# Kernel optimization log

Measured on AMD Instinct MI355X. Metric: run time of the kernel, lower is better.

The kernel has to match this reference:

```python
import jax, jax.numpy as jnp
import numpy as np
import math

NDIM = 16
SCALE = math.sqrt(1.0 / NDIM)


def setup_inputs() -> dict:
    key = jax.random.key(0)
    ks = jax.random.split(key, 7)
    L, Bsz, Dm = 4096, 4, 1024
    return {
        "x": jax.random.normal(ks[0], (L, Bsz, Dm), dtype=jnp.float32),
        "log_dt": jax.random.normal(ks[1], (Dm, 1), dtype=jnp.float32),
        "log_A_real": jax.random.normal(ks[2], (Dm, NDIM), dtype=jnp.float32),
        "A_imag": jax.random.normal(ks[3], (Dm, NDIM), dtype=jnp.float32),
        "B": jax.random.normal(ks[4], (Dm, NDIM, 2), dtype=jnp.float32),
        "C": jax.random.normal(ks[5], (Dm, NDIM, 2), dtype=jnp.float32),
        "D_param": jax.random.normal(ks[6], (Dm,), dtype=jnp.float32),
    }


def _compute_kernel(log_dt, log_A_real, A_imag, B, C, length):
    dt = jnp.exp(log_dt)                                  # (D,1)
    A = -jnp.exp(log_A_real) + 1j * A_imag                # (D,N) complex
    dtA = A * dt                                          # (D,N)
    Cc = (B[..., 0] + 1j * B[..., 1]) * (C[..., 0] + 1j * C[..., 1])  # (D,N)
    # bilinear discretization
    p = Cc * dt / (1.0 - dtA / 2)                         # (D,N)
    log_q = jnp.log((1.0 + dtA / 2) / (1.0 - dtA / 2))    # (D,N)
    # Vandermonde: (D,N,L) complex — the kernel-gen bottleneck
    vander = jnp.exp(jnp.arange(length)[None, None, :] * log_q[:, :, None])
    k = jnp.einsum('dnl,dn->dl', vander, p * SCALE).real  # (D,L)
    return k


def reference(x, log_dt, log_A_real, A_imag, B, C, D_param):
    seq_len, bsz, dim = x.shape
    residual = x * D_param                                # (L,B,D)
    xt = jnp.transpose(x, (1, 2, 0))                      # (B,D,L)
    k = _compute_kernel(log_dt, log_A_real, A_imag, B, C, seq_len)
    fft_len = 2 * seq_len
    k_f = jnp.fft.rfft(k.astype(jnp.float32), n=fft_len)  # (D, fft_len//2+1)
    x_f = jnp.fft.rfft(xt.astype(jnp.float32), n=fft_len)  # (B,D, fft_len//2+1)
    out = jnp.fft.irfft(x_f * k_f, n=fft_len)[..., :seq_len]  # (B,D,L)
    out = out.astype(x.dtype)
    return jax.nn.silu(jnp.transpose(out, (2, 0, 1)) + residual)
```

## Files before the change

### kernel.cpp

```cpp
#include <hip/hip_runtime.h>
#include <math.h>

#define L_SEQ  4096
#define BSZ    4
#define DM     1024
#define NS     16
#define NCHUNK 64
#define CHUNK  (L_SEQ / NCHUNK)
#define LOG2_CHUNK 6
#define SCALE  0.25f


__global__ void s4d_params(const float* __restrict__ log_dt,
                           const float* __restrict__ log_A_real,
                           const float* __restrict__ A_imag,
                           const float* __restrict__ Bp,
                           const float* __restrict__ Cp,
                           float4* __restrict__ pq) {
    int t = blockIdx.x * blockDim.x + threadIdx.x;
    if (t >= DM * NS) return;
    int d = t >> 4;
    float dt = expf(log_dt[d]);
    float Ar = -expf(log_A_real[t]);
    float Ai = A_imag[t];
    float ar = 0.5f * Ar * dt, ai = 0.5f * Ai * dt;
    float den_r = 1.0f - ar, den_i = -ai;
    float num_r = 1.0f + ar, num_i = ai;
    float inv = 1.0f / (den_r * den_r + den_i * den_i);
    float qr = (num_r * den_r + num_i * den_i) * inv;
    float qi = (num_i * den_r - num_r * den_i) * inv;
    float B0 = Bp[2 * t], B1 = Bp[2 * t + 1];
    float C0 = Cp[2 * t], C1 = Cp[2 * t + 1];
    float ccr = B0 * C0 - B1 * C1;
    float cci = B0 * C1 + B1 * C0;
    float s = dt * inv * SCALE;
    float pr = (ccr * den_r + cci * den_i) * s;
    float pi = (cci * den_r - ccr * den_i) * s;
    pq[t] = make_float4(qr, qi, pr, pi);
}

__global__ __launch_bounds__(256, 4)
void s4d_pass1(const float* __restrict__ x,
               const float4* __restrict__ pq,
               float2* __restrict__ S) {
    int tid = blockIdx.x * 256 + threadIdx.x;
    int d  = tid & (DM - 1);
    int bc = tid >> 10;
    int c  = bc & (NCHUNK - 1);
    int b  = bc >> LOG2_CHUNK;

    float qr[NS], qi[NS], hr[NS], hi[NS];
#pragma unroll
    for (int n = 0; n < NS; ++n) {
        float4 v = pq[d * NS + n];
        qr[n] = v.x; qi[n] = v.y; hr[n] = 0.0f; hi[n] = 0.0f;
    }
    const float* xp = x + (size_t)(c * CHUNK) * (BSZ * DM) + b * DM + d;
#pragma unroll 4
    for (int l = 0; l < CHUNK; ++l) {
        float xv = xp[(size_t)l * (BSZ * DM)];
#pragma unroll
        for (int n = 0; n < NS; ++n) {
            float nr = fmaf(qr[n], hr[n], fmaf(-qi[n], hi[n], xv));
            float ni = fmaf(qr[n], hi[n], qi[n] * hr[n]);
            hr[n] = nr; hi[n] = ni;
        }
    }
    float2* sp = S + ((size_t)bc * DM + d) * NS;
#pragma unroll
    for (int n = 0; n < NS; ++n) sp[n] = make_float2(hr[n], hi[n]);
}

__global__ void s4d_pass2(const float4* __restrict__ pq,
                          float2* __restrict__ S) {
    int tid = blockIdx.x * 256 + threadIdx.x;
    int n = tid & (NS - 1);
    int d = (tid >> 4) & (DM - 1);
    int b = tid >> 14;
    float4 v = pq[d * NS + n];
    float qr = v.x, qi = v.y;
#pragma unroll
    for (int i = 0; i < LOG2_CHUNK; ++i) {
        float nr = qr * qr - qi * qi;
        float ni = 2.0f * qr * qi;
        qr = nr; qi = ni;
    }
    float hr = 0.0f, hi = 0.0f;
    for (int c = 0; c < NCHUNK; ++c) {
        size_t idx = ((size_t)(b * NCHUNK + c) * DM + d) * NS + n;
        float2 s = S[idx];
        S[idx] = make_float2(hr, hi);
        float nr = fmaf(qr, hr, fmaf(-qi, hi, s.x));
        float ni = fmaf(qr, hi, fmaf(qi, hr, s.y));
        hr = nr; hi = ni;
    }
}

__global__ __launch_bounds__(256, 4)
void s4d_pass3(const float* __restrict__ x,
               const float* __restrict__ Dp,
               const float4* __restrict__ pq,
               const float2* __restrict__ S,
               float* __restrict__ out) {
    int tid = blockIdx.x * 256 + threadIdx.x;
    int d  = tid & (DM - 1);
    int bc = tid >> 10;
    int c  = bc & (NCHUNK - 1);
    int b  = bc >> LOG2_CHUNK;

    float qr[NS], qi[NS], pr[NS], pi[NS], hr[NS], hi[NS];
#pragma unroll
    for (int n = 0; n < NS; ++n) {
        float4 v = pq[d * NS + n];
        qr[n] = v.x; qi[n] = v.y; pr[n] = v.z; pi[n] = v.w;
    }
    const float2* sp = S + ((size_t)bc * DM + d) * NS;
#pragma unroll
    for (int n = 0; n < NS; ++n) {
        float2 s = sp[n];
        hr[n] = s.x; hi[n] = s.y;
    }
    float dpar = Dp[d];
    const float* xp = x + (size_t)(c * CHUNK) * (BSZ * DM) + b * DM + d;
    float* op = out + (size_t)(c * CHUNK) * (BSZ * DM) + b * DM + d;
#pragma unroll 4
    for (int l = 0; l < CHUNK; ++l) {
        float xv = xp[(size_t)l * (BSZ * DM)];
        float acc = 0.0f;
#pragma unroll
        for (int n = 0; n < NS; ++n) {
            float nr = fmaf(qr[n], hr[n], fmaf(-qi[n], hi[n], xv));
            float ni = fmaf(qr[n], hi[n], qi[n] * hr[n]);
            hr[n] = nr; hi[n] = ni;
            acc = fmaf(pr[n], nr, fmaf(-pi[n], ni, acc));
        }
        float z = fmaf(xv, dpar, acc);
        float sig = 1.0f / (1.0f + expf(-z));
        op[(size_t)l * (BSZ * DM)] = z * sig;
    }
}

extern "C" void kernel_launch(void* const* d_in, const int* in_sizes, int n_in,
                              void* d_out, int out_size, void* d_ws, size_t ws_size,
                              hipStream_t stream) {
    const float* x          = (const float*)d_in[0];
    const float* log_dt     = (const float*)d_in[1];
    const float* log_A_real = (const float*)d_in[2];
    const float* A_imag     = (const float*)d_in[3];
    const float* Bp         = (const float*)d_in[4];
    const float* Cp         = (const float*)d_in[5];
    const float* Dp         = (const float*)d_in[6];
    float* out = (float*)d_out;

    float4* pq = (float4*)d_ws;
    float2* S  = (float2*)((char*)d_ws + sizeof(float4) * DM * NS);

    hipLaunchKernelGGL(s4d_params, dim3((DM * NS) / 256), dim3(256), 0, stream,
                       log_dt, log_A_real, A_imag, Bp, Cp, pq);
    hipLaunchKernelGGL(s4d_pass1, dim3((BSZ * NCHUNK * DM) / 256), dim3(256), 0, stream,
                       x, pq, S);
    hipLaunchKernelGGL(s4d_pass2, dim3((BSZ * DM * NS) / 256), dim3(256), 0, stream,
                       pq, S);
    hipLaunchKernelGGL(s4d_pass3, dim3((BSZ * NCHUNK * DM) / 256), dim3(256), 0, stream,
                       x, Dp, pq, S, out);
}
```

Baseline: 224.3 us.

## Split SSM states across half-waves, transpose param/state layouts for coalescing

Each (b,chunk,d) scan in passes 1 and 3 is now split across two half-wavefronts, each handling 8 of the 16 states, with a cross-lane shuffle reducing the output contribution. Parameter and chunk-state buffers are transposed to an n-major layout so loads and stores are coalesced over d. Pass 2 gets its chunk loads batched and prefetched eight at a time. This doubles thread count and cuts per-thread register pressure and serial latency, but x is now loaded twice and half the lanes idle on the store.

```diff
diff --git a/kernel.cpp b/kernel.cpp
--- a/kernel.cpp
+++ b/kernel.cpp
@@ -5,10 +5,12 @@
 #define BSZ    4
 #define DM     1024
 #define NS     16
+#define NSH    8
 #define NCHUNK 64
 #define CHUNK  (L_SEQ / NCHUNK)
 #define LOG2_CHUNK 6
 #define SCALE  0.25f
+#define LBD    (BSZ * DM)
 
 
 __global__ void s4d_params(const float* __restrict__ log_dt,
@@ -16,127 +18,169 @@
                            const float* __restrict__ A_imag,
                            const float* __restrict__ Bp,
                            const float* __restrict__ Cp,
-                           float4* __restrict__ pq) {
+                           float2* __restrict__ qbuf,
+                           float2* __restrict__ pbuf) {
     int t = blockIdx.x * blockDim.x + threadIdx.x;
-    if (t >= DM * NS) return;
-    int d = t >> 4;
+    if (t >= NS * DM) return;
+    int n = t >> 10, d = t & (DM - 1);
+    int i = d * NS + n;
     float dt = expf(log_dt[d]);
-    float Ar = -expf(log_A_real[t]);
-    float Ai = A_imag[t];
+    float Ar = -expf(log_A_real[i]);
+    float Ai = A_imag[i];
     float ar = 0.5f * Ar * dt, ai = 0.5f * Ai * dt;
     float den_r = 1.0f - ar, den_i = -ai;
     float num_r = 1.0f + ar, num_i = ai;
     float inv = 1.0f / (den_r * den_r + den_i * den_i);
     float qr = (num_r * den_r + num_i * den_i) * inv;
     float qi = (num_i * den_r - num_r * den_i) * inv;
-    float B0 = Bp[2 * t], B1 = Bp[2 * t + 1];
-    float C0 = Cp[2 * t], C1 = Cp[2 * t + 1];
+    float B0 = Bp[2 * i], B1 = Bp[2 * i + 1];
+    float C0 = Cp[2 * i], C1 = Cp[2 * i + 1];
     float ccr = B0 * C0 - B1 * C1;
     float cci = B0 * C1 + B1 * C0;
     float s = dt * inv * SCALE;
     float pr = (ccr * den_r + cci * den_i) * s;
     float pi = (cci * den_r - ccr * den_i) * s;
-    pq[t] = make_float4(qr, qi, pr, pi);
+    qbuf[t] = make_float2(qr, qi);
+    pbuf[t] = make_float2(pr, pi);
 }
 
 __global__ __launch_bounds__(256, 4)
 void s4d_pass1(const float* __restrict__ x,
-               const float4* __restrict__ pq,
+               const float2* __restrict__ qbuf,
+               float2* __restrict__ S) {
+    int tid  = blockIdx.x * 256 + threadIdx.x;
+    int lane = tid & 63;
+    int dlo  = lane & 31;
+    int half = lane >> 5;
+    int u    = tid >> 6;
+    int dhi  = u & 31;
+    int bc   = u >> 5;
+    int c    = bc & (NCHUNK - 1);
+    int d    = dhi * 32 + dlo;
+    int b    = bc >> LOG2_CHUNK;
+    int nb   = half * NSH;
+
+    float qr[NSH], qi[NSH], hr[NSH], hi[NSH];
+#pragma unroll
+    for (int j = 0; j < NSH; ++j) {
+        float2 v = qbuf[(nb + j) * DM + d];
+        qr[j] = v.x; qi[j] = v.y; hr[j] = 0.0f; hi[j] = 0.0f;
+    }
+    const float* xp = x + (size_t)(c * CHUNK) * LBD + b * DM + d;
+#pragma unroll 4
+    for (int l = 0; l < CHUNK; ++l) {
+        float xv = xp[(size_t)l * LBD];
+#pragma unroll
+        for (int j = 0; j < NSH; ++j) {
+            float nr = fmaf(qr[j], hr[j], fmaf(-qi[j], hi[j], xv));
+            float ni = fmaf(qr[j], hi[j], qi[j] * hr[j]);
+            hr[j] = nr; hi[j] = ni;
+        }
+    }
+    float2* sp = S + ((size_t)bc * NS + nb) * DM + d;
+#pragma unroll
+    for (int j = 0; j < NSH; ++j) sp[(size_t)j * DM] = make_float2(hr[j], hi[j]);
+}
+
+__global__ __launch_bounds__(256)
+void s4d_pass2(const float2* __restrict__ qbuf,
                float2* __restrict__ S) {
     int tid = blockIdx.x * 256 + threadIdx.x;
-    int d  = tid & (DM - 1);
-    int bc = tid >> 10;
-    int c  = bc & (NCHUNK - 1);
-    int b  = bc >> LOG2_CHUNK;
-
-    float qr[NS], qi[NS], hr[NS], hi[NS];
-#pragma unroll
-    for (int n = 0; n < NS; ++n) {
-        float4 v = pq[d * NS + n];
-        qr[n] = v.x; qi[n] = v.y; hr[n] = 0.0f; hi[n] = 0.0f;
-    }
-    const float* xp = x + (size_t)(c * CHUNK) * (BSZ * DM) + b * DM + d;
-#pragma unroll 4
-    for (int l = 0; l < CHUNK; ++l) {
-        float xv = xp[(size_t)l * (BSZ * DM)];
-#pragma unroll
-        for (int n = 0; n < NS; ++n) {
-            float nr = fmaf(qr[n], hr[n], fmaf(-qi[n], hi[n], xv));
-            float ni = fmaf(qr[n], hi[n], qi[n] * hr[n]);
-            hr[n] = nr; hi[n] = ni;
-        }
-    }
-    float2* sp = S + ((size_t)bc * DM + d) * NS;
-#pragma unroll
-    for (int n = 0; n < NS; ++n) sp[n] = make_float2(hr[n], hi[n]);
-}
-
-__global__ void s4d_pass2(const float4* __restrict__ pq,
-                          float2* __restrict__ S) {
-    int tid = blockIdx.x * 256 + threadIdx.x;
-    int n = tid & (NS - 1);
-    int d = (tid >> 4) & (DM - 1);
+    int d = tid & (DM - 1);
+    int n = (tid >> 10) & (NS - 1);
     int b = tid >> 14;
-    float4 v = pq[d * NS + n];
-    float qr = v.x, qi = v.y;
+    float2 qv = qbuf[n * DM + d];
+    float qr = qv.x, qi = qv.y;
 #pragma unroll
     for (int i = 0; i < LOG2_CHUNK; ++i) {
         float nr = qr * qr - qi * qi;
         float ni = 2.0f * qr * qi;
         qr = nr; qi = ni;
     }
+    size_t base = ((size_t)b * NCHUNK * NS + n) * DM + d;
+    const size_t cs = (size_t)NS * DM;
     float hr = 0.0f, hi = 0.0f;
-    for (int c = 0; c < NCHUNK; ++c) {
-        size_t idx = ((size_t)(b * NCHUNK + c) * DM + d) * NS + n;
-        float2 s = S[idx];
-        S[idx] = make_float2(hr, hi);
-        float nr = fmaf(qr, hr, fmaf(-qi, hi, s.x));
-        float ni = fmaf(qr, hi, fmaf(qi, hr, s.y));
-        hr = nr; hi = ni;
+    float2 s0 = S[base + 0 * cs], s1 = S[base + 1 * cs],
+           s2 = S[base + 2 * cs], s3 = S[base + 3 * cs],
+           s4 = S[base + 4 * cs], s5 = S[base + 5 * cs],
+           s6 = S[base + 6 * cs], s7 = S[base + 7 * cs];
+#pragma unroll
+    for (int c0 = 0; c0 < NCHUNK; c0 += 8) {
+        float2 t0, t1, t2, t3, t4, t5, t6, t7;
+        if (c0 + 8 < NCHUNK) {
+            size_t nb2 = base + (size_t)(c0 + 8) * cs;
+            t0 = S[nb2 + 0 * cs]; t1 = S[nb2 + 1 * cs];
+            t2 = S[nb2 + 2 * cs]; t3 = S[nb2 + 3 * cs];
+            t4 = S[nb2 + 4 * cs]; t5 = S[nb2 + 5 * cs];
+            t6 = S[nb2 + 6 * cs]; t7 = S[nb2 + 7 * cs];
+        }
+#define STEP(J, SB)                                                      \
+        {                                                                \
+            S[base + (size_t)(c0 + J) * cs] = make_float2(hr, hi);       \
+            float nr = fmaf(qr, hr, fmaf(-qi, hi, SB.x));                \
+            float ni = fmaf(qr, hi, fmaf(qi, hr, SB.y));                 \
+            hr = nr; hi = ni;                                            \
+        }
+        STEP(0, s0) STEP(1, s1) STEP(2, s2) STEP(3, s3)
+        STEP(4, s4) STEP(5, s5) STEP(6, s6) STEP(7, s7)
+#undef STEP
+        if (c0 + 8 < NCHUNK) {
+            s0 = t0; s1 = t1; s2 = t2; s3 = t3;
+            s4 = t4; s5 = t5; s6 = t6; s7 = t7;
+        }
     }
 }
 
 __global__ __launch_bounds__(256, 4)
 void s4d_pass3(const float* __restrict__ x,
                const float* __restrict__ Dp,
-               const float4* __restrict__ pq,
+               const float2* __restrict__ qbuf,
+               const float2* __restrict__ pbuf,
                const float2* __restrict__ S,
                float* __restrict__ out) {
-    int tid = blockIdx.x * 256 + threadIdx.x;
-    int d  = tid & (DM - 1);
-    int bc = tid >> 10;
-    int c  = bc & (NCHUNK - 1);
-    int b  = bc >> LOG2_CHUNK;
-
-    float qr[NS], qi[NS], pr[NS], pi[NS], hr[NS], hi[NS];
-#pragma unroll
-    for (int n = 0; n < NS; ++n) {
-        float4 v = pq[d * NS + n];
-        qr[n] = v.x; qi[n] = v.y; pr[n] = v.z; pi[n] = v.w;
-    }
-    const float2* sp = S + ((size_t)bc * DM + d) * NS;
-#pragma unroll
-    for (int n = 0; n < NS; ++n) {
-        float2 s = sp[n];
-        hr[n] = s.x; hi[n] = s.y;
+    int tid  = blockIdx.x * 256 + threadIdx.x;
+    int lane = tid & 63;
+    int dlo  = lane & 31;
+    int half = lane >> 5;
+    int u    = tid >> 6;
+    int dhi  = u & 31;
+    int bc   = u >> 5;
+    int c    = bc & (NCHUNK - 1);
+    int d    = dhi * 32 + dlo;
+    int b    = bc >> LOG2_CHUNK;
+    int nb   = half * NSH;
+
+    float qr[NSH], qi[NSH], pr[NSH], pi[NSH], hr[NSH], hi[NSH];
+#pragma unroll
+    for (int j = 0; j < NSH; ++j) {
+        float2 v = qbuf[(nb + j) * DM + d];
+        float2 w = pbuf[(nb + j) * DM + d];
+        qr[j] = v.x; qi[j] = v.y; pr[j] = w.x; pi[j] = w.y;
+    }
+    const float2* sp = S + ((size_t)bc * NS + nb) * DM + d;
+#pragma unroll
+    for (int j = 0; j < NSH; ++j) {
+        float2 s = sp[(size_t)j * DM];
+        hr[j] = s.x; hi[j] = s.y;
     }
     float dpar = Dp[d];
-    const float* xp = x + (size_t)(c * CHUNK) * (BSZ * DM) + b * DM + d;
-    float* op = out + (size_t)(c * CHUNK) * (BSZ * DM) + b * DM + d;
-#pragma unroll 4
+    const float* xp = x + (size_t)(c * CHUNK) * LBD + b * DM + d;
+    float* op = out + (size_t)(c * CHUNK) * LBD + b * DM + d;
+#pragma unroll 2
     for (int l = 0; l < CHUNK; ++l) {
-        float xv = xp[(size_t)l * (BSZ * DM)];
+        float xv = xp[(size_t)l * LBD];
         float acc = 0.0f;
 #pragma unroll
-        for (int n = 0; n < NS; ++n) {
-            float nr = fmaf(qr[n], hr[n], fmaf(-qi[n], hi[n], xv));
-            float ni = fmaf(qr[n], hi[n], qi[n] * hr[n]);
-            hr[n] = nr; hi[n] = ni;
-            acc = fmaf(pr[n], nr, fmaf(-pi[n], ni, acc));
-        }
+        for (int j = 0; j < NSH; ++j) {
+            float nr = fmaf(qr[j], hr[j], fmaf(-qi[j], hi[j], xv));
+            float ni = fmaf(qr[j], hi[j], qi[j] * hr[j]);
+            hr[j] = nr; hi[j] = ni;
+            acc = fmaf(pr[j], nr, fmaf(-pi[j], ni, acc));
+        }
+        acc += __shfl_xor(acc, 32, 64);
         float z = fmaf(xv, dpar, acc);
         float sig = 1.0f / (1.0f + expf(-z));
-        op[(size_t)l * (BSZ * DM)] = z * sig;
+        if (half == 0) op[(size_t)l * LBD] = z * sig;
     }
 }
 
@@ -152,15 +196,16 @@
     const float* Dp         = (const float*)d_in[6];
     float* out = (float*)d_out;
 
-    float4* pq = (float4*)d_ws;
-    float2* S  = (float2*)((char*)d_ws + sizeof(float4) * DM * NS);
-
-    hipLaunchKernelGGL(s4d_params, dim3((DM * NS) / 256), dim3(256), 0, stream,
-                       log_dt, log_A_real, A_imag, Bp, Cp, pq);
-    hipLaunchKernelGGL(s4d_pass1, dim3((BSZ * NCHUNK * DM) / 256), dim3(256), 0, stream,
-                       x, pq, S);
+    float2* qbuf = (float2*)d_ws;
+    float2* pbuf = qbuf + NS * DM;
+    float2* S    = pbuf + NS * DM;
+
+    hipLaunchKernelGGL(s4d_params, dim3((NS * DM) / 256), dim3(256), 0, stream,
+                       log_dt, log_A_real, A_imag, Bp, Cp, qbuf, pbuf);
+    hipLaunchKernelGGL(s4d_pass1, dim3((2 * BSZ * NCHUNK * DM) / 256), dim3(256), 0, stream,
+                       x, qbuf, S);
     hipLaunchKernelGGL(s4d_pass2, dim3((BSZ * DM * NS) / 256), dim3(256), 0, stream,
-                       pq, S);
-    hipLaunchKernelGGL(s4d_pass3, dim3((BSZ * NCHUNK * DM) / 256), dim3(256), 0, stream,
-                       x, Dp, pq, S, out);
-}
+                       qbuf, S);
+    hipLaunchKernelGGL(s4d_pass3, dim3((2 * BSZ * NCHUNK * DM) / 256), dim3(256), 0, stream,
+                       x, Dp, qbuf, pbuf, S, out);
+}
```

Result: faster. 219.5 us (-2.2%).
